# Kernel tuning notes

Hardware: AMD Instinct MI355X
Metric: run time of the kernel (lower is better)

## Reference

```python
import jax, jax.numpy as jnp
import numpy as np

MIN_SIZE = 25.0      # remove_small_boxes threshold (init default)
IOU_THRESH = 0.3     # nms iou_threshold (init default)
MAX_DET = 100        # rcnn_detections_per_image (init default)
IMG = 1024.0         # synthetic image size for box generation


def setup_inputs() -> dict:
    key = jax.random.key(0)
    k1, k2, k3 = jax.random.split(key, 3)
    B, N = 16, 4096
    # valid xyxy boxes inside a 1024x1024 image
    cxcy = jax.random.uniform(k1, (B, N, 2), minval=0.0, maxval=IMG)
    wh = jax.random.uniform(k2, (B, N, 2), minval=1.0, maxval=300.0)
    boxes = jnp.concatenate([cxcy - wh / 2, cxcy + wh / 2], axis=-1)
    boxes = jnp.clip(boxes, 0.0, IMG)
    scores = jax.random.uniform(k3, (B, N))
    return {"boxes": boxes, "scores": scores}


def _pairwise_iou(b):
    # b: [N,4] xyxy -> iou: [N,N]
    area = (b[:, 2] - b[:, 0]) * (b[:, 3] - b[:, 1])
    lt = jnp.maximum(b[:, None, :2], b[None, :, :2])
    rb = jnp.minimum(b[:, None, 2:], b[None, :, 2:])
    wh = jnp.clip(rb - lt, 0.0)
    inter = wh[..., 0] * wh[..., 1]
    return inter / (area[:, None] + area[None, :] - inter + 1e-9)


def _per_image(boxes, scores):
    # boxes [N,4], scores [N] -> (out_boxes [K,4], valid [K])
    N = boxes.shape[0]
    # remove_small_boxes: width and height >= min_size
    valid = ((boxes[:, 2] - boxes[:, 0]) >= MIN_SIZE) & ((boxes[:, 3] - boxes[:, 1]) >= MIN_SIZE)
    s = jnp.where(valid, scores, -jnp.inf)
    order = jnp.argsort(-s)          # score-descending, invalid boxes last
    b = boxes[order]
    v = valid[order]
    iou = _pairwise_iou(b)           # [N,N] dominant intermediate
    idx = jnp.arange(N)

    def body(i, keep):
        # greedy NMS: box i (if kept) suppresses lower-scored overlapping boxes
        sup = (iou[i] > IOU_THRESH) & keep[i] & (idx > i)
        return keep & ~sup

    keep = jax.lax.fori_loop(0, N, body, v)
    # first MAX_DET kept boxes in score order (fixed-shape top-k truncation)
    sel = jnp.argsort(jnp.where(keep, idx, N))[:MAX_DET]
    valid_out = jnp.take(keep, sel)
    out_boxes = jnp.where(valid_out[:, None], b[sel], 0.0)
    return out_boxes, valid_out


def reference(boxes, scores):
    # boxes [B,N,4], scores [B,N] -> [B,K,5] rows (image_idx, x1,y1,x2,y2);
    # padded rows have image_idx = -1 (fixed-shape analogue of the ragged concat)
    out_boxes, valid = jax.vmap(_per_image)(boxes, scores)
    B = boxes.shape[0]
    img_idx = jnp.where(valid, jnp.arange(B, dtype=boxes.dtype)[:, None], -1.0)
    return jnp.concatenate([img_idx[..., None], out_boxes], axis=-1)
```

## Files before the change

kernel.cpp:

```cpp
#include <hip/hip_runtime.h>
#include <math.h>

#define N_BOX 4096
#define B_IMG 16
#define MAXDET 100
#define MINSZ 25.0f
#define IOUT 0.3f
#define IG 16
#define JG 8
#define JW (N_BOX / JG)

__device__ __forceinline__ float iou_f(float ax1, float ay1, float ax2, float ay2, float aarea,
                                       float bx1, float by1, float bx2, float by2, float barea) {
#pragma clang fp contract(off)
    float lx = fmaxf(ax1, bx1);
    float ly = fmaxf(ay1, by1);
    float rx = fminf(ax2, bx2);
    float ry = fminf(ay2, by2);
    float wx = fmaxf(rx - lx, 0.0f);
    float wy = fmaxf(ry - ly, 0.0f);
    float inter = wx * wy;
    float denom = ((aarea + barea) - inter) + 1e-9f;
    return inter / denom;
}

__global__ __launch_bounds__(256) void key_kernel(
        const float4* __restrict__ boxes, const float* __restrict__ scores,
        unsigned long long* __restrict__ ckey) {
    int idx = blockIdx.x * 256 + threadIdx.x;
    float4 bx = boxes[idx];
    bool valid = ((bx.z - bx.x) >= MINSZ) && ((bx.w - bx.y) >= MINSZ);
    float k = valid ? scores[idx] : -INFINITY;
    unsigned u = __float_as_uint(k);
    u = (u & 0x80000000u) ? ~u : (u | 0x80000000u);
    int i = idx & (N_BOX - 1);
    ckey[idx] = ((unsigned long long)u << 12) | (unsigned long long)(N_BOX - 1 - i);
}

__global__ __launch_bounds__(256) void partial_rank_kernel(
        const unsigned long long* __restrict__ ckey, unsigned short* __restrict__ part) {
    int blk = blockIdx.x;
    int jg = blk & (JG - 1);
    int ig = (blk >> 3) & (IG - 1);
    int b  = blk >> 7;
    int t = threadIdx.x;
    int i = ig * 256 + t;
    unsigned long long ci = ckey[b * N_BOX + i];
    const unsigned long long* cj = ckey + b * N_BOX + jg * JW;
    int r = 0;
#pragma unroll 8
    for (int j = 0; j < JW; ++j)
        r += (cj[j] > ci) ? 1 : 0;
    part[(b * JG + jg) * N_BOX + i] = (unsigned short)r;
}

__global__ __launch_bounds__(256) void scatter_kernel(
        const unsigned long long* __restrict__ ckey,
        const unsigned short* __restrict__ part,
        unsigned short* __restrict__ inv) {
    int idx = blockIdx.x * 256 + threadIdx.x;
    int b = idx >> 12;
    int i = idx & (N_BOX - 1);
    int rank = 0;
#pragma unroll
    for (int jg = 0; jg < JG; ++jg)
        rank += part[(b * JG + jg) * N_BOX + i];
    unsigned valid = (unsigned)(ckey[idx] >> 43) & 1u;
    inv[b * N_BOX + rank] = (unsigned short)(i | (valid << 15));
}

__global__ __launch_bounds__(64) void nms_kernel(
        const float4* __restrict__ boxes, const unsigned short* __restrict__ inv,
        float* __restrict__ out) {
    __shared__ float kx1[192], ky1[192], kx2[192], ky2[192], kar[192];
    int b = blockIdx.x;
    int l = threadIdx.x;
    const float4* bb = boxes + (size_t)b * N_BOX;
    const unsigned short* iv = inv + (size_t)b * N_BOX;

    int keptCnt = 0;
    unsigned short ni = iv[l];
    float4 nbx = bb[ni & 0xFFFu];
    for (int c = 0; c < 64; ++c) {
        unsigned short e = ni;
        float4 bx = nbx;
        if (c < 63) { ni = iv[(c + 1) * 64 + l]; nbx = bb[ni & 0xFFFu]; }
        float x1 = bx.x, y1 = bx.y, x2 = bx.z, y2 = bx.w;
        float ar;
        {
#pragma clang fp contract(off)
            ar = (x2 - x1) * (y2 - y1);
        }
        bool alive = (e >> 15) != 0;
        for (int q = 0; q < keptCnt; ++q) {
            float v = iou_f(kx1[q], ky1[q], kx2[q], ky2[q], kar[q],
                            x1, y1, x2, y2, ar);
            if (v > IOUT) alive = false;
        }
        unsigned long long m = __ballot(alive);
        unsigned long long mm = m;
        while (mm) {
            int i = __ffsll(mm) - 1;
            float bx1 = __shfl(x1, i), by1 = __shfl(y1, i);
            float bx2 = __shfl(x2, i), by2 = __shfl(y2, i);
            float ba  = __shfl(ar, i);
            float v = iou_f(bx1, by1, bx2, by2, ba, x1, y1, x2, y2, ar);
            bool sup = (l > i) && (v > IOUT) && ((m >> l) & 1ull);
            unsigned long long sm = __ballot(sup);
            m &= ~sm;
            mm &= ~(1ull << i);
            mm &= m;
        }
        int cnt = __popcll(m);
        int pos = keptCnt + __popcll(m & ((1ull << l) - 1ull));
        if ((m >> l) & 1ull) {
            kx1[pos] = x1; ky1[pos] = y1; kx2[pos] = x2; ky2[pos] = y2; kar[pos] = ar;
        }
        keptCnt += cnt;
        __syncthreads();
        if (keptCnt >= MAXDET) break;
    }

    int tot = keptCnt < MAXDET ? keptCnt : MAXDET;
    float* ob = out + (size_t)b * MAXDET * 5;
    for (int r = l; r < MAXDET; r += 64) {
        float* row = ob + r * 5;
        if (r < tot) {
            row[0] = (float)b;
            row[1] = kx1[r]; row[2] = ky1[r]; row[3] = kx2[r]; row[4] = ky2[r];
        } else {
            row[0] = -1.0f;
            row[1] = 0.0f; row[2] = 0.0f; row[3] = 0.0f; row[4] = 0.0f;
        }
    }
}

extern "C" void kernel_launch(void* const* d_in, const int* in_sizes, int n_in,
                              void* d_out, int out_size, void* d_ws, size_t ws_size,
                              hipStream_t stream) {
    const float4* boxes = (const float4*)d_in[0];
    const float* scores = (const float*)d_in[1];
    float* out = (float*)d_out;

    unsigned long long* ckey = (unsigned long long*)d_ws;
    unsigned short* part     = (unsigned short*)((char*)d_ws + (size_t)524288);
    unsigned short* inv      = (unsigned short*)((char*)d_ws + (size_t)1572864);

    key_kernel<<<B_IMG * N_BOX / 256, 256, 0, stream>>>(boxes, scores, ckey);
    partial_rank_kernel<<<B_IMG * IG * JG, 256, 0, stream>>>(ckey, part);
    scatter_kernel<<<B_IMG * N_BOX / 256, 256, 0, stream>>>(ckey, part, inv);
    nms_kernel<<<B_IMG, 64, 0, stream>>>(boxes, inv, out);
}
```

Measured before the change: 110.2 us.

## Fuse key, partial-rank and scatter kernels into one LDS-based rank kernel

Result: slower. 146.3 us (+32.7%).

```diff
diff --git a/kernel.cpp b/kernel.cpp
--- a/kernel.cpp
+++ b/kernel.cpp
@@ -6,9 +6,6 @@
 #define MAXDET 100
 #define MINSZ 25.0f
 #define IOUT 0.3f
-#define IG 16
-#define JG 8
-#define JW (N_BOX / JG)
 
 __device__ __forceinline__ float iou_f(float ax1, float ay1, float ax2, float ay2, float aarea,
                                        float bx1, float by1, float bx2, float by2, float barea) {
@@ -24,49 +21,41 @@
     return inter / denom;
 }
 
-__global__ __launch_bounds__(256) void key_kernel(
+__global__ __launch_bounds__(256) void rank_kernel(
         const float4* __restrict__ boxes, const float* __restrict__ scores,
-        unsigned long long* __restrict__ ckey) {
-    int idx = blockIdx.x * 256 + threadIdx.x;
-    float4 bx = boxes[idx];
-    bool valid = ((bx.z - bx.x) >= MINSZ) && ((bx.w - bx.y) >= MINSZ);
-    float k = valid ? scores[idx] : -INFINITY;
-    unsigned u = __float_as_uint(k);
-    u = (u & 0x80000000u) ? ~u : (u | 0x80000000u);
-    int i = idx & (N_BOX - 1);
-    ckey[idx] = ((unsigned long long)u << 12) | (unsigned long long)(N_BOX - 1 - i);
-}
+        unsigned short* __restrict__ inv) {
+    __shared__ __align__(16) unsigned long long keys[N_BOX];
+    int blk = blockIdx.x;
+    int b  = blk >> 4;
+    int ig = blk & 15;
+    int t = threadIdx.x;
+    const float4* bb = boxes + (size_t)b * N_BOX;
+    const float* ss = scores + (size_t)b * N_BOX;
 
-__global__ __launch_bounds__(256) void partial_rank_kernel(
-        const unsigned long long* __restrict__ ckey, unsigned short* __restrict__ part) {
-    int blk = blockIdx.x;
-    int jg = blk & (JG - 1);
-    int ig = (blk >> 3) & (IG - 1);
-    int b  = blk >> 7;
-    int t = threadIdx.x;
+#pragma unroll
+    for (int p = 0; p < 16; ++p) {
+        int j = t + 256 * p;
+        float4 bx = bb[j];
+        bool valid = ((bx.z - bx.x) >= MINSZ) && ((bx.w - bx.y) >= MINSZ);
+        float k = valid ? ss[j] : -INFINITY;
+        unsigned u = __float_as_uint(k);
+        u = (u & 0x80000000u) ? ~u : (u | 0x80000000u);
+        keys[j] = ((unsigned long long)u << 12) | (unsigned long long)(N_BOX - 1 - j);
+    }
+    __syncthreads();
+
     int i = ig * 256 + t;
-    unsigned long long ci = ckey[b * N_BOX + i];
-    const unsigned long long* cj = ckey + b * N_BOX + jg * JW;
+    unsigned long long ci = keys[i];
+    const ulonglong2* k2 = (const ulonglong2*)keys;
     int r = 0;
-#pragma unroll 8
-    for (int j = 0; j < JW; ++j)
-        r += (cj[j] > ci) ? 1 : 0;
-    part[(b * JG + jg) * N_BOX + i] = (unsigned short)r;
-}
-
-__global__ __launch_bounds__(256) void scatter_kernel(
-        const unsigned long long* __restrict__ ckey,
-        const unsigned short* __restrict__ part,
-        unsigned short* __restrict__ inv) {
-    int idx = blockIdx.x * 256 + threadIdx.x;
-    int b = idx >> 12;
-    int i = idx & (N_BOX - 1);
-    int rank = 0;
-#pragma unroll
-    for (int jg = 0; jg < JG; ++jg)
-        rank += part[(b * JG + jg) * N_BOX + i];
-    unsigned valid = (unsigned)(ckey[idx] >> 43) & 1u;
-    inv[b * N_BOX + rank] = (unsigned short)(i | (valid << 15));
+#pragma unroll 4
+    for (int j2 = 0; j2 < N_BOX / 2; ++j2) {
+        ulonglong2 kk = k2[j2];
+        r += (kk.x > ci) ? 1 : 0;
+        r += (kk.y > ci) ? 1 : 0;
+    }
+    unsigned valid = (unsigned)(ci >> 43) & 1u;
+    inv[b * N_BOX + r] = (unsigned short)(i | (valid << 15));
 }
 
 __global__ __launch_bounds__(64) void nms_kernel(
@@ -142,12 +131,8 @@
     const float* scores = (const float*)d_in[1];
     float* out = (float*)d_out;
 
-    unsigned long long* ckey = (unsigned long long*)d_ws;
-    unsigned short* part     = (unsigned short*)((char*)d_ws + (size_t)524288);
-    unsigned short* inv      = (unsigned short*)((char*)d_ws + (size_t)1572864);
+    unsigned short* inv = (unsigned short*)d_ws;
 
-    key_kernel<<<B_IMG * N_BOX / 256, 256, 0, stream>>>(boxes, scores, ckey);
-    partial_rank_kernel<<<B_IMG * IG * JG, 256, 0, stream>>>(ckey, part);
-    scatter_kernel<<<B_IMG * N_BOX / 256, 256, 0, stream>>>(ckey, part, inv);
+    rank_kernel<<<B_IMG * 16, 256, 0, stream>>>(boxes, scores, inv);
     nms_kernel<<<B_IMG, 64, 0, stream>>>(boxes, inv, out);
 }
```

## Process four NMS chunks per group with four wavefronts in the NMS kernel

Applied to the files above, without the earlier changes.

Result: no change. 111.9 us (+1.5%).

```diff
diff --git a/kernel.cpp b/kernel.cpp
--- a/kernel.cpp
+++ b/kernel.cpp
@@ -69,22 +69,22 @@
     inv[b * N_BOX + rank] = (unsigned short)(i | (valid << 15));
 }
 
-__global__ __launch_bounds__(64) void nms_kernel(
+__global__ __launch_bounds__(256) void nms_kernel(
         const float4* __restrict__ boxes, const unsigned short* __restrict__ inv,
         float* __restrict__ out) {
-    __shared__ float kx1[192], ky1[192], kx2[192], ky2[192], kar[192];
+    __shared__ __align__(16) float4 kbox[384];
+    __shared__ int scnt[4];
     int b = blockIdx.x;
-    int l = threadIdx.x;
+    int t = threadIdx.x;
+    int w = t >> 6, l = t & 63;
     const float4* bb = boxes + (size_t)b * N_BOX;
     const unsigned short* iv = inv + (size_t)b * N_BOX;
 
-    int keptCnt = 0;
-    unsigned short ni = iv[l];
-    float4 nbx = bb[ni & 0xFFFu];
-    for (int c = 0; c < 64; ++c) {
-        unsigned short e = ni;
-        float4 bx = nbx;
-        if (c < 63) { ni = iv[(c + 1) * 64 + l]; nbx = bb[ni & 0xFFFu]; }
+    int kept = 0;
+    for (int g = 0; g < 16; ++g) {
+        int c = g * 4 + w;
+        unsigned short e = iv[c * 64 + l];
+        float4 bx = bb[e & 0xFFFu];
         float x1 = bx.x, y1 = bx.y, x2 = bx.z, y2 = bx.w;
         float ar;
         {
@@ -92,42 +92,68 @@
             ar = (x2 - x1) * (y2 - y1);
         }
         bool alive = (e >> 15) != 0;
-        for (int q = 0; q < keptCnt; ++q) {
-            float v = iou_f(kx1[q], ky1[q], kx2[q], ky2[q], kar[q],
-                            x1, y1, x2, y2, ar);
+        int K0 = kept;
+        for (int q = 0; q < K0; ++q) {
+            float4 kb = kbox[q];
+            float kar;
+            {
+#pragma clang fp contract(off)
+                kar = (kb.z - kb.x) * (kb.w - kb.y);
+            }
+            float v = iou_f(kb.x, kb.y, kb.z, kb.w, kar, x1, y1, x2, y2, ar);
             if (v > IOUT) alive = false;
         }
-        unsigned long long m = __ballot(alive);
-        unsigned long long mm = m;
-        while (mm) {
-            int i = __ffsll(mm) - 1;
-            float bx1 = __shfl(x1, i), by1 = __shfl(y1, i);
-            float bx2 = __shfl(x2, i), by2 = __shfl(y2, i);
-            float ba  = __shfl(ar, i);
-            float v = iou_f(bx1, by1, bx2, by2, ba, x1, y1, x2, y2, ar);
-            bool sup = (l > i) && (v > IOUT) && ((m >> l) & 1ull);
-            unsigned long long sm = __ballot(sup);
-            m &= ~sm;
-            mm &= ~(1ull << i);
-            mm &= m;
+        for (int s = 0; s < 4; ++s) {
+            if (w == s) {
+                int Kcur = K0;
+                for (int ss = 0; ss < s; ++ss) Kcur += scnt[ss];
+                int cnt = 0;
+                if (Kcur < MAXDET) {
+                    for (int q = K0; q < Kcur; ++q) {
+                        float4 kb = kbox[q];
+                        float kar;
+                        {
+#pragma clang fp contract(off)
+                            kar = (kb.z - kb.x) * (kb.w - kb.y);
+                        }
+                        float v = iou_f(kb.x, kb.y, kb.z, kb.w, kar, x1, y1, x2, y2, ar);
+                        if (v > IOUT) alive = false;
+                    }
+                    unsigned long long m = __ballot(alive);
+                    unsigned long long mm = m;
+                    while (mm) {
+                        int i = __ffsll(mm) - 1;
+                        float bx1 = __shfl(x1, i), by1 = __shfl(y1, i);
+                        float bx2 = __shfl(x2, i), by2 = __shfl(y2, i);
+                        float ba  = __shfl(ar, i);
+                        float v = iou_f(bx1, by1, bx2, by2, ba, x1, y1, x2, y2, ar);
+                        bool sup = (l > i) && (v > IOUT) && ((m >> l) & 1ull);
+                        unsigned long long sm = __ballot(sup);
+                        m &= ~sm;
+                        mm &= ~(1ull << i);
+                        mm &= m;
+                    }
+                    cnt = __popcll(m);
+                    int pos = Kcur + __popcll(m & ((1ull << l) - 1ull));
+                    if ((m >> l) & 1ull) kbox[pos] = make_float4(x1, y1, x2, y2);
+                }
+                if (l == 0) scnt[s] = cnt;
+            }
+            __syncthreads();
         }
-        int cnt = __popcll(m);
-        int pos = keptCnt + __popcll(m & ((1ull << l) - 1ull));
-        if ((m >> l) & 1ull) {
-            kx1[pos] = x1; ky1[pos] = y1; kx2[pos] = x2; ky2[pos] = y2; kar[pos] = ar;
-        }
-        keptCnt += cnt;
+        kept = K0 + scnt[0] + scnt[1] + scnt[2] + scnt[3];
         __syncthreads();
-        if (keptCnt >= MAXDET) break;
+        if (kept >= MAXDET) break;
     }
 
-    int tot = keptCnt < MAXDET ? keptCnt : MAXDET;
+    int tot = kept < MAXDET ? kept : MAXDET;
     float* ob = out + (size_t)b * MAXDET * 5;
-    for (int r = l; r < MAXDET; r += 64) {
+    for (int r = t; r < MAXDET; r += 256) {
         float* row = ob + r * 5;
         if (r < tot) {
+            float4 kb = kbox[r];
             row[0] = (float)b;
-            row[1] = kx1[r]; row[2] = ky1[r]; row[3] = kx2[r]; row[4] = ky2[r];
+            row[1] = kb.x; row[2] = kb.y; row[3] = kb.z; row[4] = kb.w;
         } else {
             row[0] = -1.0f;
             row[1] = 0.0f; row[2] = 0.0f; row[3] = 0.0f; row[4] = 0.0f;
@@ -149,5 +175,5 @@
     key_kernel<<<B_IMG * N_BOX / 256, 256, 0, stream>>>(boxes, scores, ckey);
     partial_rank_kernel<<<B_IMG * IG * JG, 256, 0, stream>>>(ckey, part);
     scatter_kernel<<<B_IMG * N_BOX / 256, 256, 0, stream>>>(ckey, part, inv);
-    nms_kernel<<<B_IMG, 64, 0, stream>>>(boxes, inv, out);
+    nms_kernel<<<B_IMG, 256, 0, stream>>>(boxes, inv, out);
 }
```
